# Kernel tuning notes

Measured on AMD Instinct MI355X. Metric: run time of the kernel, lower is better.

The kernel has to match this reference:

```python
import jax, jax.numpy as jnp
import numpy as np

VOCAB, HIDDEN = 128, 1024
BATCH, SEQ = 64, 512


def setup_inputs() -> dict:
    key = jax.random.key(0)
    ks = jax.random.split(key, 6)
    scale = 1.0 / np.sqrt(HIDDEN)
    return {
        "x": jax.random.randint(ks[0], (BATCH, SEQ), 0, VOCAB, dtype=jnp.int32),
        "h": jnp.zeros((BATCH, HIDDEN), dtype=jnp.float32),
        "emb": jax.random.normal(ks[1], (VOCAB, HIDDEN), dtype=jnp.float32),
        "W_hx": jax.random.normal(ks[2], (HIDDEN, HIDDEN), dtype=jnp.float32) * scale,
        "b_hx": jnp.zeros((HIDDEN,), dtype=jnp.float32),
        "W_hh": jax.random.normal(ks[3], (HIDDEN, HIDDEN), dtype=jnp.float32) * scale,
        "W_out": jax.random.normal(ks[4], (HIDDEN, VOCAB), dtype=jnp.float32) * scale,
        "b_out": jnp.zeros((VOCAB,), dtype=jnp.float32),
    }


def reference(x, h, emb, W_hx, b_hx, W_hh, W_out, b_out):
    # x: [B, S] int indices; h: [B, H] initial hidden state
    x_emb = emb[x]  # [B, S, H] embedding lookup

    def step(h, xt):  # xt: [B, H]
        h_new = jnp.tanh(xt @ W_hx + b_hx + h @ W_hh)
        return h_new, h_new

    # scan over time axis (sequential dependency on h)
    h_final, hs = jax.lax.scan(step, h, jnp.swapaxes(x_emb, 0, 1))  # hs: [S, B, H]
    out = jnp.swapaxes(hs, 0, 1)  # [B, S, H]
    logits = out @ W_out + b_out  # [B, S, V]
    return logits, h_final
```

## Files before the change

### kernel.cpp

```cpp
#include <hip/hip_runtime.h>
#include <stdint.h>
#include <stddef.h>

#define VOCAB  128
#define HIDDEN 1024
#define BATCH  64
#define SEQ    512

#define NGROUP 4
#define BG     16
#define NWG    32
#define CJ     32
#define NVW    4
#define NTHR   512

#define E2_OFF   0
#define WOT_OFF  131072
#define HPH_OFF  262144
#define HPL_OFF  327680
#define FLG_OFF  393216

typedef __attribute__((ext_vector_type(8))) short short8_t;
typedef __attribute__((ext_vector_type(4))) float f32x4;

__device__ __forceinline__ uint4 cload4u(const void* p) {
    uint4 v;
    asm volatile("global_load_dwordx4 %0, %1, off sc0 sc1" : "=v"(v) : "v"(p));
    return v;
}
__device__ __forceinline__ int cloadi(const int* p) {
    int v;
    asm volatile("global_load_dword %0, %1, off sc0 sc1\n\ts_waitcnt vmcnt(0)"
                 : "=v"(v) : "v"(p) : "memory");
    return v;
}
__device__ __forceinline__ void cstore_short(void* p, unsigned int x) {
    asm volatile("global_store_short %0, %1, off sc0 sc1" :: "v"(p), "v"(x) : "memory");
}
__device__ __forceinline__ void cstorei(int* p, int x) {
    asm volatile("global_store_dword %0, %1, off sc0 sc1" :: "v"(p), "v"(x) : "memory");
}
#define WAITVM0() asm volatile("s_waitcnt vmcnt(0)" ::: "memory")

__device__ __forceinline__ unsigned short bf16_rne(float f) {
    unsigned int u = __float_as_uint(f);
    u += 0x7FFF + ((u >> 16) & 1);
    return (unsigned short)(u >> 16);
}
__device__ __forceinline__ float bf16_f32(unsigned short h) {
    return __uint_as_float(((unsigned int)h) << 16);
}

__global__ void e2_kernel(const float* __restrict__ emb, const float* __restrict__ W_hx,
                          const float* __restrict__ b_hx, float* __restrict__ E2) {
    int v = blockIdx.x >> 2;
    int j = (blockIdx.x & 3) * 256 + threadIdx.x;
    const float* er = emb + (size_t)v * HIDDEN;
    float acc = 0.f;
#pragma unroll 8
    for (int k = 0; k < HIDDEN; ++k)
        acc += er[k] * W_hx[(size_t)k * HIDDEN + j];
    E2[(size_t)v * HIDDEN + j] = acc + b_hx[j];
}

__global__ void wot_kernel(const float* __restrict__ W_out, float* __restrict__ WoT) {
    int v  = blockIdx.x;
    int k4 = threadIdx.x;
    float4 r;
    r.x = W_out[(size_t)(k4*4+0)*VOCAB + v];
    r.y = W_out[(size_t)(k4*4+1)*VOCAB + v];
    r.z = W_out[(size_t)(k4*4+2)*VOCAB + v];
    r.w = W_out[(size_t)(k4*4+3)*VOCAB + v];
    ((float4*)(WoT + (size_t)v * HIDDEN))[k4] = r;
}

extern "C" __global__ void __launch_bounds__(NTHR, 2)
rnn_kernel(const int* __restrict__ x, const float* __restrict__ h0,
           const float* __restrict__ W_hh,
           const float* __restrict__ E2, const float* __restrict__ WoT,
           const float* __restrict__ b_out,
           unsigned short* __restrict__ hpHi, unsigned short* __restrict__ hpLo,
           int* __restrict__ flags,
           float* __restrict__ logits, float* __restrict__ hf) {
    extern __shared__ char lds_raw[];
    short* sHi  = (short*)lds_raw;
    short* sLo  = sHi + 16 * 1024;
    float* sPart = (float*)(sLo + 16 * 1024);
    int*   sX   = (int*)(sPart + 8 * 512);

    const int wg = blockIdx.x;
    const int g  = wg / NWG;
    const int w  = wg % NWG;
    const int b0 = g * BG;
    const int j0 = w * CJ;
    const int tid  = threadIdx.x;
    const int lane = tid & 63;
    const int wv   = tid >> 6;
    int* flg = flags + (((size_t)g) << 9);

    {
        const int4* xs4 = (const int4*)(x + (size_t)b0 * SEQ);
#pragma unroll
        for (int i = 0; i < 4; ++i)
            ((int4*)sX)[tid + 512 * i] = xs4[tid + 512 * i];
    }

    short8_t whi[2][4], wlo[2][4];
    {
        const int colb = lane & 15, kgrp = lane >> 4;
#pragma unroll
        for (int ct = 0; ct < 2; ++ct) {
            int col = j0 + ct * 16 + colb;
#pragma unroll
            for (int c = 0; c < 4; ++c) {
                int kb = wv * 128 + c * 32 + kgrp * 8;
#pragma unroll
                for (int e = 0; e < 8; ++e) {
                    float wval = W_hh[(size_t)(kb + e) * HIDDEN + col];
                    unsigned short hi = bf16_rne(wval);
                    whi[ct][c][e] = (short)hi;
                    wlo[ct][c][e] = (short)bf16_rne(wval - bf16_f32(hi));
                }
            }
        }
    }

    short8_t wvo[4];
    {
        const int colv = lane & 15, kgrp = lane >> 4;
#pragma unroll
        for (int c = 0; c < 4; ++c) {
            int kb = wv * 128 + c * 32 + kgrp * 8;
#pragma unroll
            for (int e = 0; e < 8; ++e) {
                float wval = (colv < NVW) ? WoT[(size_t)(w * NVW + colv) * HIDDEN + kb + e] : 0.f;
                wvo[c][e] = (short)bf16_rne(wval);
            }
        }
    }
    const float boV = (tid < 64) ? b_out[w * NVW + (tid & 3)] : 0.f;
    __syncthreads();

    const int srow = tid >> 5;
    const int sslt = tid & 31;
    const int rb = tid >> 5, jb = tid & 31;
    const int ar = lane & 15, acg = lane >> 4;

    for (int t = 0; t < SEQ; ++t) {
        if (t > 0) {
            if (tid < 64) {
                int guard = 0;
                while (guard < (1 << 24)) {
                    int v = cloadi(flg + ((lane & 31) << 4));
                    if (__all(v >= t)) break;
                    __builtin_amdgcn_s_sleep(1);
                    ++guard;
                }
            }
            __syncthreads();
        }

        float e2p;
        if (t == 0) {
#pragma unroll
            for (int i = 0; i < 4; ++i) {
                int c = i * 32 + sslt;
                const float* p = h0 + (size_t)(b0 + srow) * HIDDEN + c * 8;
                short8_t h8, l8;
#pragma unroll
                for (int e = 0; e < 8; ++e) {
                    float vv = p[e];
                    unsigned short hi = bf16_rne(vv);
                    h8[e] = (short)hi;
                    l8[e] = (short)bf16_rne(vv - bf16_f32(hi));
                }
                int cs = (c ^ (srow & 7)) << 3;
                *(short8_t*)(sHi + srow * 1024 + cs) = h8;
                *(short8_t*)(sLo + srow * 1024 + cs) = l8;
            }
            e2p = E2[(size_t)sX[rb * SEQ + t] * HIDDEN + j0 + jb];
        } else {
            const unsigned short* srcH = hpHi + (size_t)((t - 1) & 1) * BATCH * HIDDEN
                                              + (size_t)(b0 + srow) * HIDDEN;
            const unsigned short* srcL = hpLo + (size_t)((t - 1) & 1) * BATCH * HIDDEN
                                              + (size_t)(b0 + srow) * HIDDEN;
            uint4 th[4], tl[4];
#pragma unroll
            for (int i = 0; i < 4; ++i) {
                int c = i * 32 + sslt;
                th[i] = cload4u(srcH + c * 8);
                tl[i] = cload4u(srcL + c * 8);
            }
            e2p = E2[(size_t)sX[rb * SEQ + t] * HIDDEN + j0 + jb];
            WAITVM0();
            __builtin_amdgcn_sched_barrier(0);
#pragma unroll
            for (int i = 0; i < 4; ++i) {
                int c = i * 32 + sslt;
                int cs = (c ^ (srow & 7)) << 3;
                *(uint4*)(sHi + srow * 1024 + cs) = th[i];
                *(uint4*)(sLo + srow * 1024 + cs) = tl[i];
            }
        }
        __syncthreads();

        f32x4 acc0 = {0.f, 0.f, 0.f, 0.f};
        f32x4 acc1 = {0.f, 0.f, 0.f, 0.f};
#pragma unroll
        for (int c = 0; c < 4; ++c) {
            int c8 = wv * 16 + c * 4 + acg;
            int off = ar * 1024 + ((c8 ^ (ar & 7)) << 3);
            short8_t ahi = *(const short8_t*)(sHi + off);
            short8_t alo = *(const short8_t*)(sLo + off);
            acc0 = __builtin_amdgcn_mfma_f32_16x16x32_bf16(ahi, whi[0][c], acc0, 0, 0, 0);
            acc1 = __builtin_amdgcn_mfma_f32_16x16x32_bf16(ahi, whi[1][c], acc1, 0, 0, 0);
            acc0 = __builtin_amdgcn_mfma_f32_16x16x32_bf16(alo, whi[0][c], acc0, 0, 0, 0);
            acc1 = __builtin_amdgcn_mfma_f32_16x16x32_bf16(alo, whi[1][c], acc1, 0, 0, 0);
            acc0 = __builtin_amdgcn_mfma_f32_16x16x32_bf16(ahi, wlo[0][c], acc0, 0, 0, 0);
            acc1 = __builtin_amdgcn_mfma_f32_16x16x32_bf16(ahi, wlo[1][c], acc1, 0, 0, 0);
        }
#pragma unroll
        for (int q = 0; q < 4; ++q) {
            sPart[wv * 512 + (acg * 4 + q) * 32 + ar]      = acc0[q];
            sPart[wv * 512 + (acg * 4 + q) * 32 + 16 + ar] = acc1[q];
        }
        __syncthreads();

        {
            float s = 0.f;
#pragma unroll
            for (int z = 0; z < 8; ++z) s += sPart[z * 512 + tid];
            float hn = tanhf(s + e2p);
            unsigned short hi = bf16_rne(hn);
            unsigned short lo = bf16_rne(hn - bf16_f32(hi));
            size_t di = (size_t)(t & 1) * BATCH * HIDDEN + (size_t)(b0 + rb) * HIDDEN + j0 + jb;
            cstore_short(hpHi + di, hi);
            cstore_short(hpLo + di, lo);
            if (t == SEQ - 1)
                hf[(size_t)(b0 + rb) * HIDDEN + j0 + jb] = hn;
        }
        WAITVM0();
        __syncthreads();
        if (tid == 0)
            cstorei(flg + (w << 4), t + 1);

        if (t > 0) {
            f32x4 accL = {0.f, 0.f, 0.f, 0.f};
#pragma unroll
            for (int c = 0; c < 4; ++c) {
                int c8 = wv * 16 + c * 4 + acg;
                int off = ar * 1024 + ((c8 ^ (ar & 7)) << 3);
                short8_t ahi = *(const short8_t*)(sHi + off);
                accL = __builtin_amdgcn_mfma_f32_16x16x32_bf16(ahi, wvo[c], accL, 0, 0, 0);
            }
            if (ar < NVW) {
#pragma unroll
                for (int q = 0; q < 4; ++q)
                    sPart[wv * 64 + (acg * 4 + q) * 4 + ar] = accL[q];
            }
            __syncthreads();
            if (tid < 64) {
                int b = tid >> 2, v = tid & 3;
                float s = 0.f;
#pragma unroll
                for (int z = 0; z < 8; ++z) s += sPart[z * 64 + b * 4 + v];
                logits[((size_t)(b0 + b) * SEQ + (t - 1)) * VOCAB + w * NVW + v] = s + boV;
            }
        }
    }

    if (tid < 64) {
        int guard = 0;
        while (guard < (1 << 24)) {
            int v = cloadi(flg + ((lane & 31) << 4));
            if (__all(v >= SEQ)) break;
            __builtin_amdgcn_s_sleep(1);
            ++guard;
        }
    }
    __syncthreads();
    {
        const unsigned short* srcH = hpHi + (size_t)((SEQ - 1) & 1) * BATCH * HIDDEN
                                          + (size_t)(b0 + srow) * HIDDEN;
#pragma unroll
        for (int i = 0; i < 4; ++i) {
            int c = i * 32 + sslt;
            uint4 th = cload4u(srcH + c * 8);
            WAITVM0();
            int cs = (c ^ (srow & 7)) << 3;
            *(uint4*)(sHi + srow * 1024 + cs) = th;
        }
    }
    __syncthreads();
    {
        f32x4 accL = {0.f, 0.f, 0.f, 0.f};
#pragma unroll
        for (int c = 0; c < 4; ++c) {
            int c8 = wv * 16 + c * 4 + acg;
            int off = ar * 1024 + ((c8 ^ (ar & 7)) << 3);
            short8_t ahi = *(const short8_t*)(sHi + off);
            accL = __builtin_amdgcn_mfma_f32_16x16x32_bf16(ahi, wvo[c], accL, 0, 0, 0);
        }
        if (ar < NVW) {
#pragma unroll
            for (int q = 0; q < 4; ++q)
                sPart[wv * 64 + (acg * 4 + q) * 4 + ar] = accL[q];
        }
        __syncthreads();
        if (tid < 64) {
            int b = tid >> 2, v = tid & 3;
            float s = 0.f;
#pragma unroll
            for (int z = 0; z < 8; ++z) s += sPart[z * 64 + b * 4 + v];
            logits[((size_t)(b0 + b) * SEQ + (SEQ - 1)) * VOCAB + w * NVW + v] = s + boV;
        }
    }
}

extern "C" void kernel_launch(void* const* d_in, const int* in_sizes, int n_in,
                              void* d_out, int out_size, void* d_ws, size_t ws_size,
                              hipStream_t stream) {
    (void)in_sizes; (void)n_in; (void)out_size; (void)ws_size;
    const int*   x     = (const int*)  d_in[0];
    const float* h0    = (const float*)d_in[1];
    const float* emb   = (const float*)d_in[2];
    const float* W_hx  = (const float*)d_in[3];
    const float* b_hx  = (const float*)d_in[4];
    const float* W_hh  = (const float*)d_in[5];
    const float* W_out = (const float*)d_in[6];
    const float* b_out = (const float*)d_in[7];

    float* logits = (float*)d_out;
    float* hf     = logits + (size_t)BATCH * SEQ * VOCAB;

    float* ws  = (float*)d_ws;
    float* E2  = ws + E2_OFF;
    float* WoT = ws + WOT_OFF;
    unsigned short* hpHi = (unsigned short*)(ws + HPH_OFF);
    unsigned short* hpLo = (unsigned short*)(ws + HPL_OFF);
    int*   flags = (int*)(ws + FLG_OFF);

    hipMemsetAsync(flags, 0, NGROUP * 32 * 64, stream);
    e2_kernel<<<512, 256, 0, stream>>>(emb, W_hx, b_hx, E2);
    wot_kernel<<<128, 256, 0, stream>>>(W_out, WoT);

    hipFuncSetAttribute(reinterpret_cast<const void*>(rnn_kernel),
                        hipFuncAttributeMaxDynamicSharedMemorySize, 114688);
    rnn_kernel<<<NGROUP * NWG, NTHR, 114688, stream>>>(x, h0, W_hh, E2, WoT, b_out,
                                                       hpHi, hpLo, flags, logits, hf);
}
```

Baseline: 1.707 ms.

## Replace flag-based step barrier with poison-sentinel data polling on packed hidden buffers

Drops the per-group flag counters and the store-wait-syncthreads-flag sequence. Each step now writes packed hi/lo bf16 hidden values into a four-slot ring and re-poisons the slot two steps ahead. Consumers poll the data itself until no word equals the poison value, which removes one global round trip and a block barrier from every recurrent step. The cost is double-width polling loads and a reliance on the poison bit pattern never appearing as a real hi/lo value; WoT is also pre-converted to bf16 in its own kernel.

```diff
diff --git a/kernel.cpp b/kernel.cpp
--- a/kernel.cpp
+++ b/kernel.cpp
@@ -14,11 +14,11 @@
 #define NVW    4
 #define NTHR   512
 
+#define POISON 0x7F800000u
+
 #define E2_OFF   0
 #define WOT_OFF  131072
-#define HPH_OFF  262144
-#define HPL_OFF  327680
-#define FLG_OFF  393216
+#define BUF_OFF  196608
 
 typedef __attribute__((ext_vector_type(8))) short short8_t;
 typedef __attribute__((ext_vector_type(4))) float f32x4;
@@ -28,19 +28,11 @@
     asm volatile("global_load_dwordx4 %0, %1, off sc0 sc1" : "=v"(v) : "v"(p));
     return v;
 }
-__device__ __forceinline__ int cloadi(const int* p) {
-    int v;
-    asm volatile("global_load_dword %0, %1, off sc0 sc1\n\ts_waitcnt vmcnt(0)"
-                 : "=v"(v) : "v"(p) : "memory");
-    return v;
-}
-__device__ __forceinline__ void cstore_short(void* p, unsigned int x) {
-    asm volatile("global_store_short %0, %1, off sc0 sc1" :: "v"(p), "v"(x) : "memory");
-}
-__device__ __forceinline__ void cstorei(int* p, int x) {
+__device__ __forceinline__ void cstoreu(unsigned int* p, unsigned int x) {
     asm volatile("global_store_dword %0, %1, off sc0 sc1" :: "v"(p), "v"(x) : "memory");
 }
 #define WAITVM0() asm volatile("s_waitcnt vmcnt(0)" ::: "memory")
+#define SCHED_FENCE() __builtin_amdgcn_sched_barrier(0)
 
 __device__ __forceinline__ unsigned short bf16_rne(float f) {
     unsigned int u = __float_as_uint(f);
@@ -63,24 +55,28 @@
     E2[(size_t)v * HIDDEN + j] = acc + b_hx[j];
 }
 
-__global__ void wot_kernel(const float* __restrict__ W_out, float* __restrict__ WoT) {
+__global__ void wot_kernel(const float* __restrict__ W_out, unsigned short* __restrict__ WoT) {
     int v  = blockIdx.x;
     int k4 = threadIdx.x;
-    float4 r;
-    r.x = W_out[(size_t)(k4*4+0)*VOCAB + v];
-    r.y = W_out[(size_t)(k4*4+1)*VOCAB + v];
-    r.z = W_out[(size_t)(k4*4+2)*VOCAB + v];
-    r.w = W_out[(size_t)(k4*4+3)*VOCAB + v];
-    ((float4*)(WoT + (size_t)v * HIDDEN))[k4] = r;
+    ushort4 r;
+    r.x = bf16_rne(W_out[(size_t)(k4*4+0)*VOCAB + v]);
+    r.y = bf16_rne(W_out[(size_t)(k4*4+1)*VOCAB + v]);
+    r.z = bf16_rne(W_out[(size_t)(k4*4+2)*VOCAB + v]);
+    r.w = bf16_rne(W_out[(size_t)(k4*4+3)*VOCAB + v]);
+    ((ushort4*)(WoT + (size_t)v * HIDDEN))[k4] = r;
+}
+
+__global__ void poison_kernel(unsigned int* __restrict__ bufs) {
+    int i = blockIdx.x * 256 + threadIdx.x;
+    ((uint4*)bufs)[i] = make_uint4(POISON, POISON, POISON, POISON);
 }
 
 extern "C" __global__ void __launch_bounds__(NTHR, 2)
 rnn_kernel(const int* __restrict__ x, const float* __restrict__ h0,
            const float* __restrict__ W_hh,
-           const float* __restrict__ E2, const float* __restrict__ WoT,
+           const float* __restrict__ E2, const unsigned short* __restrict__ WoT,
            const float* __restrict__ b_out,
-           unsigned short* __restrict__ hpHi, unsigned short* __restrict__ hpLo,
-           int* __restrict__ flags,
+           unsigned int* __restrict__ bufs,
            float* __restrict__ logits, float* __restrict__ hf) {
     extern __shared__ char lds_raw[];
     short* sHi  = (short*)lds_raw;
@@ -96,7 +92,6 @@
     const int tid  = threadIdx.x;
     const int lane = tid & 63;
     const int wv   = tid >> 6;
-    int* flg = flags + (((size_t)g) << 9);
 
     {
         const int4* xs4 = (const int4*)(x + (size_t)b0 * SEQ);
@@ -132,10 +127,9 @@
         for (int c = 0; c < 4; ++c) {
             int kb = wv * 128 + c * 32 + kgrp * 8;
 #pragma unroll
-            for (int e = 0; e < 8; ++e) {
-                float wval = (colv < NVW) ? WoT[(size_t)(w * NVW + colv) * HIDDEN + kb + e] : 0.f;
-                wvo[c][e] = (short)bf16_rne(wval);
-            }
+            for (int e = 0; e < 8; ++e)
+                wvo[c][e] = (colv < NVW)
+                    ? (short)WoT[(size_t)(w * NVW + colv) * HIDDEN + kb + e] : (short)0;
         }
     }
     const float boV = (tid < 64) ? b_out[w * NVW + (tid & 3)] : 0.f;
@@ -147,20 +141,7 @@
     const int ar = lane & 15, acg = lane >> 4;
 
     for (int t = 0; t < SEQ; ++t) {
-        if (t > 0) {
-            if (tid < 64) {
-                int guard = 0;
-                while (guard < (1 << 24)) {
-                    int v = cloadi(flg + ((lane & 31) << 4));
-                    if (__all(v >= t)) break;
-                    __builtin_amdgcn_s_sleep(1);
-                    ++guard;
-                }
-            }
-            __syncthreads();
-        }
-
-        float e2p;
+        float e2p = E2[(size_t)sX[rb * SEQ + t] * HIDDEN + j0 + jb];
         if (t == 0) {
 #pragma unroll
             for (int i = 0; i < 4; ++i) {
@@ -178,28 +159,50 @@
                 *(short8_t*)(sHi + srow * 1024 + cs) = h8;
                 *(short8_t*)(sLo + srow * 1024 + cs) = l8;
             }
-            e2p = E2[(size_t)sX[rb * SEQ + t] * HIDDEN + j0 + jb];
         } else {
-            const unsigned short* srcH = hpHi + (size_t)((t - 1) & 1) * BATCH * HIDDEN
-                                              + (size_t)(b0 + srow) * HIDDEN;
-            const unsigned short* srcL = hpLo + (size_t)((t - 1) & 1) * BATCH * HIDDEN
-                                              + (size_t)(b0 + srow) * HIDDEN;
-            uint4 th[4], tl[4];
-#pragma unroll
-            for (int i = 0; i < 4; ++i) {
-                int c = i * 32 + sslt;
-                th[i] = cload4u(srcH + c * 8);
-                tl[i] = cload4u(srcL + c * 8);
-            }
-            e2p = E2[(size_t)sX[rb * SEQ + t] * HIDDEN + j0 + jb];
-            WAITVM0();
-            __builtin_amdgcn_sched_barrier(0);
+            const unsigned int* src = bufs + ((size_t)((t - 1) & 3) << 16)
+                                           + ((size_t)(b0 + srow) << 10);
+            uint4 d[8];
+            unsigned pend = 0xF;
+            int guard = 0;
+            do {
+#pragma unroll
+                for (int i = 0; i < 4; ++i)
+                    if (pend & (1u << i)) {
+                        int c = i * 32 + sslt;
+                        d[2*i]   = cload4u(src + c * 8);
+                        d[2*i+1] = cload4u(src + c * 8 + 4);
+                    }
+                WAITVM0();
+                SCHED_FENCE();
+#pragma unroll
+                for (int i = 0; i < 4; ++i)
+                    if (pend & (1u << i)) {
+                        bool ok = d[2*i].x   != POISON && d[2*i].y   != POISON
+                               && d[2*i].z   != POISON && d[2*i].w   != POISON
+                               && d[2*i+1].x != POISON && d[2*i+1].y != POISON
+                               && d[2*i+1].z != POISON && d[2*i+1].w != POISON;
+                        if (ok) pend &= ~(1u << i);
+                    }
+                if (!pend) break;
+                __builtin_amdgcn_s_sleep(1);
+            } while (++guard < (1 << 20));
+            SCHED_FENCE();
 #pragma unroll
             for (int i = 0; i < 4; ++i) {
                 int c = i * 32 + sslt;
                 int cs = (c ^ (srow & 7)) << 3;
-                *(uint4*)(sHi + srow * 1024 + cs) = th[i];
-                *(uint4*)(sLo + srow * 1024 + cs) = tl[i];
+                short8_t h8, l8;
+                h8[0]=(short)(d[2*i].x>>16);   l8[0]=(short)(d[2*i].x&0xFFFF);
+                h8[1]=(short)(d[2*i].y>>16);   l8[1]=(short)(d[2*i].y&0xFFFF);
+                h8[2]=(short)(d[2*i].z>>16);   l8[2]=(short)(d[2*i].z&0xFFFF);
+                h8[3]=(short)(d[2*i].w>>16);   l8[3]=(short)(d[2*i].w&0xFFFF);
+                h8[4]=(short)(d[2*i+1].x>>16); l8[4]=(short)(d[2*i+1].x&0xFFFF);
+                h8[5]=(short)(d[2*i+1].y>>16); l8[5]=(short)(d[2*i+1].y&0xFFFF);
+                h8[6]=(short)(d[2*i+1].z>>16); l8[6]=(short)(d[2*i+1].z&0xFFFF);
+                h8[7]=(short)(d[2*i+1].w>>16); l8[7]=(short)(d[2*i+1].w&0xFFFF);
+                *(short8_t*)(sHi + srow * 1024 + cs) = h8;
+                *(short8_t*)(sLo + srow * 1024 + cs) = l8;
             }
         }
         __syncthreads();
@@ -233,16 +236,14 @@
             float hn = tanhf(s + e2p);
             unsigned short hi = bf16_rne(hn);
             unsigned short lo = bf16_rne(hn - bf16_f32(hi));
-            size_t di = (size_t)(t & 1) * BATCH * HIDDEN + (size_t)(b0 + rb) * HIDDEN + j0 + jb;
-            cstore_short(hpHi + di, hi);
-            cstore_short(hpLo + di, lo);
+            unsigned int pk = ((unsigned int)hi << 16) | (unsigned int)lo;
+            size_t idx = ((size_t)(b0 + rb) << 10) + j0 + jb;
+            cstoreu(bufs + ((size_t)(t & 3) << 16) + idx, pk);
+            cstoreu(bufs + ((size_t)((t + 2) & 3) << 16) + idx, POISON);
             if (t == SEQ - 1)
                 hf[(size_t)(b0 + rb) * HIDDEN + j0 + jb] = hn;
         }
-        WAITVM0();
-        __syncthreads();
-        if (tid == 0)
-            cstorei(flg + (w << 4), t + 1);
+        __syncthreads();
 
         if (t > 0) {
             f32x4 accL = {0.f, 0.f, 0.f, 0.f};
@@ -269,26 +270,46 @@
         }
     }
 
-    if (tid < 64) {
+    {
+        const unsigned int* src = bufs + ((size_t)((SEQ - 1) & 3) << 16)
+                                       + ((size_t)(b0 + srow) << 10);
+        uint4 d[8];
+        unsigned pend = 0xF;
         int guard = 0;
-        while (guard < (1 << 24)) {
-            int v = cloadi(flg + ((lane & 31) << 4));
-            if (__all(v >= SEQ)) break;
+        do {
+#pragma unroll
+            for (int i = 0; i < 4; ++i)
+                if (pend & (1u << i)) {
+                    int c = i * 32 + sslt;
+                    d[2*i]   = cload4u(src + c * 8);
+                    d[2*i+1] = cload4u(src + c * 8 + 4);
+                }
+            WAITVM0();
+            SCHED_FENCE();
+#pragma unroll
+            for (int i = 0; i < 4; ++i)
+                if (pend & (1u << i)) {
+                    bool ok = d[2*i].x   != POISON && d[2*i].y   != POISON
+                           && d[2*i].z   != POISON && d[2*i].w   != POISON
+                           && d[2*i+1].x != POISON && d[2*i+1].y != POISON
+                           && d[2*i+1].z != POISON && d[2*i+1].w != POISON;
+                    if (ok) pend &= ~(1u << i);
+                }
+            if (!pend) break;
             __builtin_amdgcn_s_sleep(1);
-            ++guard;
-        }
-    }
-    __syncthreads();
-    {
-        const unsigned short* srcH = hpHi + (size_t)((SEQ - 1) & 1) * BATCH * HIDDEN
-                                          + (size_t)(b0 + srow) * HIDDEN;
+        } while (++guard < (1 << 20));
+        SCHED_FENCE();
+        __syncthreads();
 #pragma unroll
         for (int i = 0; i < 4; ++i) {
             int c = i * 32 + sslt;
-            uint4 th = cload4u(srcH + c * 8);
-            WAITVM0();
             int cs = (c ^ (srow & 7)) << 3;
-            *(uint4*)(sHi + srow * 1024 + cs) = th;
+            short8_t h8;
+            h8[0]=(short)(d[2*i].x>>16);   h8[1]=(short)(d[2*i].y>>16);
+            h8[2]=(short)(d[2*i].z>>16);   h8[3]=(short)(d[2*i].w>>16);
+            h8[4]=(short)(d[2*i+1].x>>16); h8[5]=(short)(d[2*i+1].y>>16);
+            h8[6]=(short)(d[2*i+1].z>>16); h8[7]=(short)(d[2*i+1].w>>16);
+            *(short8_t*)(sHi + srow * 1024 + cs) = h8;
         }
     }
     __syncthreads();
@@ -335,17 +356,15 @@
 
     float* ws  = (float*)d_ws;
     float* E2  = ws + E2_OFF;
-    float* WoT = ws + WOT_OFF;
-    unsigned short* hpHi = (unsigned short*)(ws + HPH_OFF);
-    unsigned short* hpLo = (unsigned short*)(ws + HPL_OFF);
-    int*   flags = (int*)(ws + FLG_OFF);
-
-    hipMemsetAsync(flags, 0, NGROUP * 32 * 64, stream);
+    unsigned short* WoT = (unsigned short*)(ws + WOT_OFF);
+    unsigned int*   bufs = (unsigned int*)(ws + BUF_OFF);
+
+    poison_kernel<<<256, 256, 0, stream>>>(bufs);
     e2_kernel<<<512, 256, 0, stream>>>(emb, W_hx, b_hx, E2);
     wot_kernel<<<128, 256, 0, stream>>>(W_out, WoT);
 
     hipFuncSetAttribute(reinterpret_cast<const void*>(rnn_kernel),
                         hipFuncAttributeMaxDynamicSharedMemorySize, 114688);
     rnn_kernel<<<NGROUP * NWG, NTHR, 114688, stream>>>(x, h0, W_hh, E2, WoT, b_out,
-                                                       hpHi, hpLo, flags, logits, hf);
-}
+                                                       bufs, logits, hf);
+}
```

New measurement: 1.653 ms. 3.2% less time.
